# Performance work log

Hardware: AMD Instinct MI355X
Metric: run time of the kernel (lower is better)

Reference implementation:

```python
import jax, jax.numpy as jnp
import numpy as np

B, D = 4096, 512
INIT_TEMP = 0.07
TEMP_MAX = 100.0


def setup_inputs() -> dict:
    key = jax.random.key(0)
    k1, k2, k3, k4 = jax.random.split(key, 4)
    return {
        "v_mean": jax.random.normal(k1, (B, D), dtype=jnp.float32),
        "v_var": jax.random.uniform(k2, (B, D), dtype=jnp.float32),
        "t_mean": jax.random.normal(k3, (B, D), dtype=jnp.float32),
        "t_var": jax.random.uniform(k4, (B, D), dtype=jnp.float32),
        "log_temp": jnp.log(jnp.asarray(1.0 / INIT_TEMP, dtype=jnp.float32)),
    }


def _pairwise_sq_dist(a, b):
    # ||a_i - b_j||^2 = ||a_i||^2 + ||b_j||^2 - 2 a_i . b_j  (GEMM expansion)
    a_sq = jnp.sum(a * a, axis=-1)            # [B]
    b_sq = jnp.sum(b * b, axis=-1)            # [B]
    cross = jnp.einsum('id,jd->ij', a, b)     # [B, B] GEMM
    return a_sq[:, None] + b_sq[None, :] - 2.0 * cross


def reference(v_mean, v_var, t_mean, t_var, log_temp):
    temperature = jnp.minimum(jnp.exp(log_temp), TEMP_MAX)
    v_sigma = jnp.sqrt(v_var)
    t_sigma = jnp.sqrt(t_var)
    # W2^2 between diagonal Gaussians (as in source: term1 + term2 only)
    w2 = _pairwise_sq_dist(v_mean, t_mean) + _pairwise_sq_dist(v_sigma, t_sigma)
    logits = -w2 * temperature                # [B, B]
    n = logits.shape[0]
    diag = jnp.arange(n)
    # CE(logits, arange): rows for image->text, columns for text->image
    logp_i = jax.nn.log_softmax(logits, axis=1)
    logp_t = jax.nn.log_softmax(logits, axis=0)
    loss_i = -jnp.mean(logp_i[diag, diag])
    loss_t = -jnp.mean(logp_t[diag, diag])
    return (loss_i + loss_t) * 0.5
```

## Files before the change

kernel.cpp:

```cpp
#include <hip/hip_runtime.h>
#include <math.h>

#define NB 4096
#define ND 512
#define K2 1024
#define NT8 8

typedef __attribute__((ext_vector_type(4))) float f32x4;
typedef __attribute__((ext_vector_type(16))) float f32x16;

__device__ __forceinline__ float wave_sum(float v) {
#pragma unroll
  for (int o = 32; o > 0; o >>= 1) v += __shfl_xor(v, o);
  return v;
}

__global__ __launch_bounds__(256) void prep_kernel(
    const float* __restrict__ v_mean, const float* __restrict__ v_var,
    const float* __restrict__ t_mean, const float* __restrict__ t_var,
    unsigned char* __restrict__ Afp, unsigned char* __restrict__ Bfp,
    float* __restrict__ a_sq, float* __restrict__ b_sq) {
  int b = blockIdx.x;
  int side = b >> 12;
  int row = b & (NB - 1);
  const float* mean = side ? t_mean : v_mean;
  const float* var = side ? t_var : v_var;
  unsigned char* dst = side ? Bfp : Afp;
  float* sq = side ? b_sq : a_sq;
  int t = threadIdx.x;
  float2 m2 = *(const float2*)(mean + (size_t)row * ND + 2 * t);
  float2 v2 = *(const float2*)(var + (size_t)row * ND + 2 * t);
  float s0 = sqrtf(v2.x), s1 = sqrtf(v2.y);
  int pm = __builtin_amdgcn_cvt_pk_fp8_f32(m2.x, m2.y, 0, false);
  int ps = __builtin_amdgcn_cvt_pk_fp8_f32(s0, s1, 0, false);
  *(unsigned short*)(dst + (size_t)row * K2 + 2 * t) = (unsigned short)(pm & 0xFFFF);
  *(unsigned short*)(dst + (size_t)row * K2 + ND + 2 * t) = (unsigned short)(ps & 0xFFFF);
  float p = m2.x * m2.x + m2.y * m2.y + v2.x + v2.y;
  p = wave_sum(p);
  __shared__ float sm[4];
  if ((t & 63) == 0) sm[t >> 6] = p;
  __syncthreads();
  if (t == 0) sq[row] = (sm[0] + sm[1]) + (sm[2] + sm[3]);
}

__global__ __launch_bounds__(512, 4) void gemm_fused_kernel(
    const unsigned char* __restrict__ Afp, const unsigned char* __restrict__ Bfp,
    const float* __restrict__ a_sq, const float* __restrict__ b_sq,
    const float* __restrict__ log_temp,
    float* __restrict__ rowM, float* __restrict__ rowS,
    float* __restrict__ colM, float* __restrict__ colS,
    float* __restrict__ diag) {
  __shared__ unsigned char ldsA[128 * 128];
  __shared__ unsigned char ldsB[256 * 128];
  int bid = blockIdx.x;
  int swz = (bid & 7) * 64 + (bid >> 3);
  int bm = swz >> 4, bn = swz & 15;
  int brow = bm * 128, bcol = bn * 256;
  int tid = threadIdx.x;
  int lane = tid & 63, wid = tid >> 6;
  int wr = wid >> 2, wc = wid & 3;
  int l31 = lane & 31, kh = lane >> 5;

  int rbase = tid >> 3, chunk = tid & 7;
  unsigned gA[2], gB[4];
  int ldA[2], ldB[4];
#pragma unroll
  for (int s = 0; s < 2; ++s) {
    int row = s * 64 + rbase;
    gA[s] = (unsigned)(brow + row) * K2 + ((chunk * 16) ^ ((row & 7) << 4));
    ldA[s] = row * 128 + chunk * 16;
  }
#pragma unroll
  for (int s = 0; s < 4; ++s) {
    int row = s * 64 + rbase;
    gB[s] = (unsigned)(bcol + row) * K2 + ((chunk * 16) ^ ((row & 7) << 4));
    ldB[s] = row * 128 + chunk * 16;
  }

#define STAGE(T)                                                               \
  {                                                                            \
    _Pragma("unroll") for (int s = 0; s < 2; ++s)                              \
        __builtin_amdgcn_global_load_lds(                                      \
            (const __attribute__((address_space(1))) unsigned int*)(Afp +      \
                gA[s] + (unsigned)(T) * 128),                                  \
            (__attribute__((address_space(3))) unsigned int*)(ldsA + ldA[s]),  \
            16, 0, 0);                                                         \
    _Pragma("unroll") for (int s = 0; s < 4; ++s)                              \
        __builtin_amdgcn_global_load_lds(                                      \
            (const __attribute__((address_space(1))) unsigned int*)(Bfp +      \
                gB[s] + (unsigned)(T) * 128),                                  \
            (__attribute__((address_space(3))) unsigned int*)(ldsB + ldB[s]),  \
            16, 0, 0);                                                         \
  }

  unsigned sw = (unsigned)(lane & 7) << 4;
  unsigned aB[2], bB[2];
#pragma unroll
  for (int mi = 0; mi < 2; ++mi)
    aB[mi] = (unsigned)(wr * 64 + mi * 32 + l31) * 128 + (unsigned)kh * 8;
#pragma unroll
  for (int ni = 0; ni < 2; ++ni)
    bB[ni] = (unsigned)(wc * 64 + ni * 32 + l31) * 128 + (unsigned)kh * 8;

  f32x16 acc[2][2] = {};

  STAGE(0);
  asm volatile("s_waitcnt vmcnt(0)" ::: "memory");
  __builtin_amdgcn_s_barrier();

  for (int t = 0; t < NT8; ++t) {
    long a0, a1, b0, b1;
#pragma unroll
    for (int ks = 0; ks < 7; ++ks) {
      unsigned ko = ((unsigned)ks << 4) ^ sw;
      a0 = *(const long*)(ldsA + aB[0] + ko);
      a1 = *(const long*)(ldsA + aB[1] + ko);
      b0 = *(const long*)(ldsB + bB[0] + ko);
      b1 = *(const long*)(ldsB + bB[1] + ko);
      __builtin_amdgcn_s_setprio(1);
      acc[0][0] = __builtin_amdgcn_mfma_f32_32x32x16_fp8_fp8(a0, b0, acc[0][0], 0, 0, 0);
      acc[0][1] = __builtin_amdgcn_mfma_f32_32x32x16_fp8_fp8(a0, b1, acc[0][1], 0, 0, 0);
      acc[1][0] = __builtin_amdgcn_mfma_f32_32x32x16_fp8_fp8(a1, b0, acc[1][0], 0, 0, 0);
      acc[1][1] = __builtin_amdgcn_mfma_f32_32x32x16_fp8_fp8(a1, b1, acc[1][1], 0, 0, 0);
      __builtin_amdgcn_s_setprio(0);
    }
    unsigned ko7 = (7u << 4) ^ sw;
    a0 = *(const long*)(ldsA + aB[0] + ko7);
    a1 = *(const long*)(ldsA + aB[1] + ko7);
    b0 = *(const long*)(ldsB + bB[0] + ko7);
    b1 = *(const long*)(ldsB + bB[1] + ko7);
    asm volatile("s_waitcnt lgkmcnt(0)" ::: "memory");
    __builtin_amdgcn_s_barrier();
    if (t + 1 < NT8) STAGE(t + 1);
    __builtin_amdgcn_s_setprio(1);
    acc[0][0] = __builtin_amdgcn_mfma_f32_32x32x16_fp8_fp8(a0, b0, acc[0][0], 0, 0, 0);
    acc[0][1] = __builtin_amdgcn_mfma_f32_32x32x16_fp8_fp8(a0, b1, acc[0][1], 0, 0, 0);
    acc[1][0] = __builtin_amdgcn_mfma_f32_32x32x16_fp8_fp8(a1, b0, acc[1][0], 0, 0, 0);
    acc[1][1] = __builtin_amdgcn_mfma_f32_32x32x16_fp8_fp8(a1, b1, acc[1][1], 0, 0, 0);
    __builtin_amdgcn_s_setprio(0);
    asm volatile("s_waitcnt vmcnt(0)" ::: "memory");
    __builtin_amdgcn_s_barrier();
  }

  float temp = fminf(expf(log_temp[0]), 100.0f);
#pragma unroll
  for (int mi = 0; mi < 2; ++mi) {
#pragma unroll
    for (int reg = 0; reg < 16; ++reg) {
      int rl = wr * 64 + mi * 32 + (reg & 3) + 8 * (reg >> 2) + 4 * kh;
      float asq = a_sq[brow + rl];
#pragma unroll
      for (int ni = 0; ni < 2; ++ni) {
        float bsq = b_sq[bcol + wc * 64 + ni * 32 + l31];
        acc[mi][ni][reg] = -temp * (asq + bsq - 2.0f * acc[mi][ni][reg]);
      }
    }
  }
  if ((bm >> 1) == bn) {
#pragma unroll
    for (int mi = 0; mi < 2; ++mi)
#pragma unroll
      for (int ni = 0; ni < 2; ++ni)
#pragma unroll
        for (int reg = 0; reg < 16; ++reg) {
          int rl = wr * 64 + mi * 32 + (reg & 3) + 8 * (reg >> 2) + 4 * kh;
          int cl = wc * 64 + ni * 32 + l31;
          if (brow + rl == bcol + cl) diag[brow + rl] = acc[mi][ni][reg];
        }
  }
#pragma unroll
  for (int mi = 0; mi < 2; ++mi) {
#pragma unroll
    for (int reg = 0; reg < 16; ++reg) {
      float mx = fmaxf(acc[mi][0][reg], acc[mi][1][reg]);
#pragma unroll
      for (int o = 1; o < 32; o <<= 1) mx = fmaxf(mx, __shfl_xor(mx, o));
      float s = __expf(acc[mi][0][reg] - mx) + __expf(acc[mi][1][reg] - mx);
#pragma unroll
      for (int o = 1; o < 32; o <<= 1) s += __shfl_xor(s, o);
      if (l31 == 0) {
        int row = brow + wr * 64 + mi * 32 + (reg & 3) + 8 * (reg >> 2) + 4 * kh;
        int ch = bn * 4 + wc;
        rowM[(size_t)row * 64 + ch] = mx;
        rowS[(size_t)row * 64 + ch] = s;
      }
    }
  }
#pragma unroll
  for (int ni = 0; ni < 2; ++ni) {
    float mx = -INFINITY;
#pragma unroll
    for (int mi = 0; mi < 2; ++mi)
#pragma unroll
      for (int reg = 0; reg < 16; ++reg) mx = fmaxf(mx, acc[mi][ni][reg]);
    mx = fmaxf(mx, __shfl_xor(mx, 32));
    float s = 0.f;
#pragma unroll
    for (int mi = 0; mi < 2; ++mi)
#pragma unroll
      for (int reg = 0; reg < 16; ++reg) s += __expf(acc[mi][ni][reg] - mx);
    s += __shfl_xor(s, 32);
    if (kh == 0) {
      int col = bcol + wc * 64 + ni * 32 + l31;
      int ch = bm * 2 + wr;
      colM[(size_t)col * 64 + ch] = mx;
      colS[(size_t)col * 64 + ch] = s;
    }
  }
}

__global__ __launch_bounds__(256) void combine_kernel(
    const float* __restrict__ rowM, const float* __restrict__ rowS,
    const float* __restrict__ colM, const float* __restrict__ colS,
    const float* __restrict__ diag, float* __restrict__ hrow,
    float* __restrict__ hcol) {
  int b = blockIdx.x;
  int t = threadIdx.x;
  int wave = t >> 6, lane = t & 63;
  int isCol = b >> 10;
  int idx = (b & 1023) * 4 + wave;
  const float* PM = isCol ? colM : rowM;
  const float* PS = isCol ? colS : rowS;
  float M = PM[(size_t)idx * 64 + lane];
  float S = PS[(size_t)idx * 64 + lane];
#pragma unroll
  for (int o = 1; o < 64; o <<= 1) {
    float M2 = __shfl_xor(M, o), S2 = __shfl_xor(S, o);
    float nM = fmaxf(M, M2);
    S = S * __expf(M - nM) + S2 * __expf(M2 - nM);
    M = nM;
  }
  if (lane == 0) {
    float v = M + logf(S) - diag[idx];
    (isCol ? hcol : hrow)[idx] = v;
  }
}

__global__ __launch_bounds__(256) void final_kernel(
    const float* __restrict__ hrow, const float* __restrict__ hcol,
    float* __restrict__ out) {
  int t = threadIdx.x;
  double a = 0.0;
  for (int i = t; i < NB; i += 256) {
    a += 0.5 * ((double)hrow[i] + (double)hcol[i]);
  }
#pragma unroll
  for (int o = 32; o > 0; o >>= 1) a += __shfl_xor(a, o);
  __shared__ double sd[4];
  if ((t & 63) == 0) sd[t >> 6] = a;
  __syncthreads();
  if (t == 0) out[0] = (float)(((sd[0] + sd[1]) + (sd[2] + sd[3])) / (double)NB);
}

extern "C" void kernel_launch(void* const* d_in, const int* in_sizes, int n_in,
                              void* d_out, int out_size, void* d_ws, size_t ws_size,
                              hipStream_t stream) {
  const float* v_mean = (const float*)d_in[0];
  const float* v_var = (const float*)d_in[1];
  const float* t_mean = (const float*)d_in[2];
  const float* t_var = (const float*)d_in[3];
  const float* log_temp = (const float*)d_in[4];
  float* out = (float*)d_out;

  char* ws = (char*)d_ws;
  unsigned char* Afp = (unsigned char*)ws;
  unsigned char* Bfp = (unsigned char*)(ws + 4194304);
  float* rowM = (float*)(ws + 8388608);
  float* rowS = rowM + (size_t)NB * 64;
  float* colM = rowS + (size_t)NB * 64;
  float* colS = colM + (size_t)NB * 64;
  float* diag = colS + (size_t)NB * 64;
  float* hrow = diag + NB;
  float* hcol = hrow + NB;
  float* a_sq = hcol + NB;
  float* b_sq = a_sq + NB;

  prep_kernel<<<8192, 256, 0, stream>>>(v_mean, v_var, t_mean, t_var, Afp, Bfp, a_sq, b_sq);
  gemm_fused_kernel<<<512, 512, 0, stream>>>(Afp, Bfp, a_sq, b_sq, log_temp,
                                             rowM, rowS, colM, colS, diag);
  combine_kernel<<<2048, 256, 0, stream>>>(rowM, rowS, colM, colS, diag, hrow, hcol);
  final_kernel<<<1, 256, 0, stream>>>(hrow, hcol, out);
}
```

Measured before the change: 64.44 us.

## Pre-tile FP8 operands into MFMA fragment order for contiguous LDS staging

```diff
diff --git a/kernel.cpp b/kernel.cpp
--- a/kernel.cpp
+++ b/kernel.cpp
@@ -8,39 +8,76 @@
 
 typedef __attribute__((ext_vector_type(4))) float f32x4;
 typedef __attribute__((ext_vector_type(16))) float f32x16;
-
-__device__ __forceinline__ float wave_sum(float v) {
-#pragma unroll
-  for (int o = 32; o > 0; o >>= 1) v += __shfl_xor(v, o);
-  return v;
-}
 
 __global__ __launch_bounds__(256) void prep_kernel(
     const float* __restrict__ v_mean, const float* __restrict__ v_var,
     const float* __restrict__ t_mean, const float* __restrict__ t_var,
     unsigned char* __restrict__ Afp, unsigned char* __restrict__ Bfp,
     float* __restrict__ a_sq, float* __restrict__ b_sq) {
-  int b = blockIdx.x;
-  int side = b >> 12;
-  int row = b & (NB - 1);
-  const float* mean = side ? t_mean : v_mean;
-  const float* var = side ? t_var : v_var;
-  unsigned char* dst = side ? Bfp : Afp;
-  float* sq = side ? b_sq : a_sq;
-  int t = threadIdx.x;
-  float2 m2 = *(const float2*)(mean + (size_t)row * ND + 2 * t);
-  float2 v2 = *(const float2*)(var + (size_t)row * ND + 2 * t);
-  float s0 = sqrtf(v2.x), s1 = sqrtf(v2.y);
-  int pm = __builtin_amdgcn_cvt_pk_fp8_f32(m2.x, m2.y, 0, false);
-  int ps = __builtin_amdgcn_cvt_pk_fp8_f32(s0, s1, 0, false);
-  *(unsigned short*)(dst + (size_t)row * K2 + 2 * t) = (unsigned short)(pm & 0xFFFF);
-  *(unsigned short*)(dst + (size_t)row * K2 + ND + 2 * t) = (unsigned short)(ps & 0xFFFF);
-  float p = m2.x * m2.x + m2.y * m2.y + v2.x + v2.y;
-  p = wave_sum(p);
-  __shared__ float sm[4];
-  if ((t & 63) == 0) sm[t >> 6] = p;
+  __shared__ __align__(16) unsigned char lfp[128 * 136];
+  int bid = blockIdx.x;
+  int tid = threadIdx.x;
+  const float* src;
+  unsigned char* dst;
+  float* sq;
+  int row0;
+  bool isVar;
+  if (bid < 256) {
+    int rb = bid >> 3, t = bid & 7;
+    row0 = rb * 128;
+    isVar = t >= 4;
+    src = (isVar ? v_var : v_mean) + (size_t)row0 * ND + (t & 3) * 128;
+    dst = Afp + (size_t)rb * 131072 + t * 16384;
+    sq = a_sq;
+  } else {
+    int b = bid - 256;
+    int rb = b >> 4, rem = b & 15, t = rem >> 1, h = rem & 1;
+    row0 = rb * 256 + h * 128;
+    isVar = t >= 4;
+    src = (isVar ? t_var : t_mean) + (size_t)row0 * ND + (t & 3) * 128;
+    dst = Bfp + (size_t)rb * 262144 + t * 32768 + h * 16384;
+    sq = b_sq;
+  }
+#pragma unroll
+  for (int q = 0; q < 16; ++q) {
+    int flat = q * 256 + tid;
+    int row = flat >> 5, c4 = flat & 31;
+    float4 v = *(const float4*)(src + row * ND + c4 * 4);
+    float p;
+    float4 w;
+    if (isVar) {
+      p = (v.x + v.y) + (v.z + v.w);
+      w.x = sqrtf(v.x); w.y = sqrtf(v.y); w.z = sqrtf(v.z); w.w = sqrtf(v.w);
+    } else {
+      p = (v.x * v.x + v.y * v.y) + (v.z * v.z + v.w * v.w);
+      w = v;
+    }
+    int p01 = __builtin_amdgcn_cvt_pk_fp8_f32(w.x, w.y, 0, false);
+    int p23 = __builtin_amdgcn_cvt_pk_fp8_f32(w.z, w.w, 0, false);
+    unsigned u = (unsigned)(p01 & 0xFFFF) | ((unsigned)(p23 & 0xFFFF) << 16);
+    *(unsigned*)(lfp + row * 136 + c4 * 4) = u;
+#pragma unroll
+    for (int o = 1; o <= 16; o <<= 1) p += __shfl_xor(p, o);
+    if ((tid & 31) == 0) atomicAdd(sq + row0 + row, p);
+  }
   __syncthreads();
-  if (t == 0) sq[row] = (sm[0] + sm[1]) + (sm[2] + sm[3]);
+  {
+    int g = tid >> 6, ks = (tid >> 3) & 7, kh = (tid >> 2) & 1;
+    int r5b = (tid & 3) * 8;
+    unsigned char* o = dst + tid * 64;
+#pragma unroll
+    for (int c = 0; c < 4; ++c) {
+      int r0 = g * 32 + r5b + c * 2;
+      unsigned long long lo =
+          *(const unsigned long long*)(lfp + r0 * 136 + ks * 16 + kh * 8);
+      unsigned long long hi =
+          *(const unsigned long long*)(lfp + (r0 + 1) * 136 + ks * 16 + kh * 8);
+      ulonglong2 v2;
+      v2.x = lo;
+      v2.y = hi;
+      *(ulonglong2*)(o + c * 16) = v2;
+    }
+  }
 }
 
 __global__ __launch_bounds__(512, 4) void gemm_fused_kernel(
@@ -61,46 +98,32 @@
   int wr = wid >> 2, wc = wid & 3;
   int l31 = lane & 31, kh = lane >> 5;
 
-  int rbase = tid >> 3, chunk = tid & 7;
-  unsigned gA[2], gB[4];
-  int ldA[2], ldB[4];
-#pragma unroll
-  for (int s = 0; s < 2; ++s) {
-    int row = s * 64 + rbase;
-    gA[s] = (unsigned)(brow + row) * K2 + ((chunk * 16) ^ ((row & 7) << 4));
-    ldA[s] = row * 128 + chunk * 16;
-  }
-#pragma unroll
-  for (int s = 0; s < 4; ++s) {
-    int row = s * 64 + rbase;
-    gB[s] = (unsigned)(bcol + row) * K2 + ((chunk * 16) ^ ((row & 7) << 4));
-    ldB[s] = row * 128 + chunk * 16;
-  }
+  const unsigned char* Ablk = Afp + (size_t)bm * 131072;
+  const unsigned char* Bblk = Bfp + (size_t)bn * 262144;
 
 #define STAGE(T)                                                               \
   {                                                                            \
     _Pragma("unroll") for (int s = 0; s < 2; ++s)                              \
         __builtin_amdgcn_global_load_lds(                                      \
-            (const __attribute__((address_space(1))) unsigned int*)(Afp +      \
-                gA[s] + (unsigned)(T) * 128),                                  \
-            (__attribute__((address_space(3))) unsigned int*)(ldsA + ldA[s]),  \
+            (const __attribute__((address_space(1))) unsigned int*)(Ablk +     \
+                (unsigned)(T) * 16384 + s * 8192 + tid * 16),                  \
+            (__attribute__((address_space(3))) unsigned int*)(ldsA + s * 8192 +\
+                tid * 16),                                                     \
             16, 0, 0);                                                         \
     _Pragma("unroll") for (int s = 0; s < 4; ++s)                              \
         __builtin_amdgcn_global_load_lds(                                      \
-            (const __attribute__((address_space(1))) unsigned int*)(Bfp +      \
-                gB[s] + (unsigned)(T) * 128),                                  \
-            (__attribute__((address_space(3))) unsigned int*)(ldsB + ldB[s]),  \
+            (const __attribute__((address_space(1))) unsigned int*)(Bblk +     \
+                (unsigned)(T) * 32768 + s * 8192 + tid * 16),                  \
+            (__attribute__((address_space(3))) unsigned int*)(ldsB + s * 8192 +\
+                tid * 16),                                                     \
             16, 0, 0);                                                         \
   }
 
-  unsigned sw = (unsigned)(lane & 7) << 4;
   unsigned aB[2], bB[2];
 #pragma unroll
-  for (int mi = 0; mi < 2; ++mi)
-    aB[mi] = (unsigned)(wr * 64 + mi * 32 + l31) * 128 + (unsigned)kh * 8;
-#pragma unroll
-  for (int ni = 0; ni < 2; ++ni)
-    bB[ni] = (unsigned)(wc * 64 + ni * 32 + l31) * 128 + (unsigned)kh * 8;
+  for (int mi = 0; mi < 2; ++mi) aB[mi] = (unsigned)(wr * 2 + mi) * 4096 + lane * 8;
+#pragma unroll
+  for (int ni = 0; ni < 2; ++ni) bB[ni] = (unsigned)(wc * 2 + ni) * 4096 + lane * 8;
 
   f32x16 acc[2][2] = {};
 
@@ -112,7 +135,7 @@
     long a0, a1, b0, b1;
 #pragma unroll
     for (int ks = 0; ks < 7; ++ks) {
-      unsigned ko = ((unsigned)ks << 4) ^ sw;
+      unsigned ko = (unsigned)ks * 512;
       a0 = *(const long*)(ldsA + aB[0] + ko);
       a1 = *(const long*)(ldsA + aB[1] + ko);
       b0 = *(const long*)(ldsB + bB[0] + ko);
@@ -124,11 +147,10 @@
       acc[1][1] = __builtin_amdgcn_mfma_f32_32x32x16_fp8_fp8(a1, b1, acc[1][1], 0, 0, 0);
       __builtin_amdgcn_s_setprio(0);
     }
-    unsigned ko7 = (7u << 4) ^ sw;
-    a0 = *(const long*)(ldsA + aB[0] + ko7);
-    a1 = *(const long*)(ldsA + aB[1] + ko7);
-    b0 = *(const long*)(ldsB + bB[0] + ko7);
-    b1 = *(const long*)(ldsB + bB[1] + ko7);
+    a0 = *(const long*)(ldsA + aB[0] + 3584);
+    a1 = *(const long*)(ldsA + aB[1] + 3584);
+    b0 = *(const long*)(ldsB + bB[0] + 3584);
+    b1 = *(const long*)(ldsB + bB[1] + 3584);
     asm volatile("s_waitcnt lgkmcnt(0)" ::: "memory");
     __builtin_amdgcn_s_barrier();
     if (t + 1 < NT8) STAGE(t + 1);
@@ -275,7 +297,8 @@
   float* a_sq = hcol + NB;
   float* b_sq = a_sq + NB;
 
-  prep_kernel<<<8192, 256, 0, stream>>>(v_mean, v_var, t_mean, t_var, Afp, Bfp, a_sq, b_sq);
+  hipMemsetAsync(a_sq, 0, 2 * (size_t)NB * sizeof(float), stream);
+  prep_kernel<<<512, 256, 0, stream>>>(v_mean, v_var, t_mean, t_var, Afp, Bfp, a_sq, b_sq);
   gemm_fused_kernel<<<512, 512, 0, stream>>>(Afp, Bfp, a_sq, b_sq, log_temp,
                                              rowM, rowS, colM, colS, diag);
   combine_kernel<<<2048, 256, 0, stream>>>(rowM, rowS, colM, colS, diag, hrow, hcol);
```

New measurement: 74.12 us. +15.0%, slower.
